# Kernel tuning notes

Hardware: AMD Instinct MI355X
Metric: run time of the kernel (lower is better)

The kernel has to match this reference:

```python
import jax, jax.numpy as jnp
import numpy as np

B, C, H, W = 2, 48, 128, 256
HEADS = 3
EPS_LN = 1e-6
EPS_NRM = 1e-12


def _conv(x, w, b, padding=0, dilation=1, groups=1):
    # x: NCHW, w: OIHW
    out = jax.lax.conv_general_dilated(
        x, w, window_strides=(1, 1),
        padding=[(padding, padding), (padding, padding)],
        rhs_dilation=(dilation, dilation),
        feature_group_count=groups,
        dimension_numbers=('NCHW', 'OIHW', 'NCHW'))
    return out + b[None, :, None, None]


def _ln2d(x, w, b):
    # LayerNorm over channel dim per pixel (NAFNet-style LayerNorm2d)
    mu = x.mean(axis=1, keepdims=True)
    var = ((x - mu) ** 2).mean(axis=1, keepdims=True)
    return (x - mu) / jnp.sqrt(var + EPS_LN) * w[None, :, None, None] + b[None, :, None, None]


def _l2norm(x):
    # F.normalize(dim=-1): x / max(||x||_2, eps)
    n = jnp.sqrt((x * x).sum(-1, keepdims=True))
    return x / jnp.maximum(n, EPS_NRM)


def setup_inputs() -> dict:
    key = jax.random.key(0)
    ks = iter(jax.random.split(key, 40))
    def nrm(shape, s=0.02):
        return jax.random.normal(next(ks), shape, jnp.float32) * s
    d = {
        'x_l': jax.random.normal(next(ks), (B, C, H, W), jnp.float32),
        'x_r': jax.random.normal(next(ks), (B, C, H, W), jnp.float32),
        'ln1_w': jnp.ones((C,), jnp.float32), 'ln1_b': jnp.zeros((C,), jnp.float32),
        'ln2_w': jnp.ones((C,), jnp.float32), 'ln2_b': jnp.zeros((C,), jnp.float32),
        'qkv_l_w': nrm((3 * C, C, 1, 1)), 'qkv_l_b': jnp.zeros((3 * C,), jnp.float32),
        'qkv_r_w': nrm((3 * C, C, 1, 1)), 'qkv_r_b': jnp.zeros((3 * C,), jnp.float32),
        'dw_l_w': nrm((3 * C, 1, 3, 3)), 'dw_l_b': jnp.zeros((3 * C,), jnp.float32),
        'dw_r_w': nrm((3 * C, 1, 3, 3)), 'dw_r_b': jnp.zeros((3 * C,), jnp.float32),
        'dil0_w': nrm((2 * C, 2 * C, 3, 3)), 'dil0_b': jnp.zeros((2 * C,), jnp.float32),
        'dil1_w': nrm((2 * C, 2 * C, 3, 3)), 'dil1_b': jnp.zeros((2 * C,), jnp.float32),
        'dil2_w': nrm((2 * C, 2 * C, 3, 3)), 'dil2_b': jnp.zeros((2 * C,), jnp.float32),
        'convQ_w': nrm((C, 6 * C, 1, 1)), 'convQ_b': jnp.zeros((C,), jnp.float32),
        'conv1_w': nrm((C, C, 1, 1)), 'conv1_b': jnp.zeros((C,), jnp.float32),
        'conv2_w': nrm((C, C, 1, 1)), 'conv2_b': jnp.zeros((C,), jnp.float32),
        'temperature': jnp.ones((HEADS, 1, 1), jnp.float32),
    }
    return d


def reference(x_l, x_r, ln1_w, ln1_b, ln2_w, ln2_b,
              qkv_l_w, qkv_l_b, qkv_r_w, qkv_r_b,
              dw_l_w, dw_l_b, dw_r_w, dw_r_b,
              dil0_w, dil0_b, dil1_w, dil1_b, dil2_w, dil2_b,
              convQ_w, convQ_b, conv1_w, conv1_b, conv2_w, conv2_b,
              temperature):
    b, c, h, w = x_l.shape
    hw = h * w
    ch = c // HEADS  # channels per head

    norm_l = _ln2d(x_l, ln1_w, ln1_b)
    norm_r = _ln2d(x_r, ln2_w, ln2_b)

    qkvl = _conv(_conv(norm_l, qkv_l_w, qkv_l_b), dw_l_w, dw_l_b, padding=1, groups=3 * c)
    qkvr = _conv(_conv(norm_r, qkv_r_w, qkv_r_b), dw_r_w, dw_r_b, padding=1, groups=3 * c)
    Q_l, K_l, V_l = jnp.split(qkvl, 3, axis=1)
    Q_r, K_r, V_r = jnp.split(qkvr, 3, axis=1)

    Q = jnp.concatenate((Q_l, Q_r), axis=1)  # [b, 2c, h, w]
    Q = jnp.concatenate((
        _conv(Q, dil0_w, dil0_b, padding=2, dilation=2),
        _conv(Q, dil1_w, dil1_b, padding=4, dilation=4),
        _conv(Q, dil2_w, dil2_b, padding=6, dilation=6)), axis=1)  # [b, 6c, h, w]
    Q = _conv(Q, convQ_w, convQ_b)  # [b, c, h, w]

    def heads(t):
        return t.reshape(b, HEADS, ch, hw)

    Q = _l2norm(heads(Q))
    K_l = _l2norm(heads(K_l))
    K_r = _l2norm(heads(K_r))
    V_l = heads(V_l)
    V_r = heads(V_r)

    # channel attention: [b, head, ch, ch]
    A_r2l = jax.nn.softmax(jnp.einsum('bhcn,bhdn->bhcd', Q, K_r) * temperature, axis=-1)
    A_l2r = jax.nn.softmax(jnp.einsum('bhcn,bhdn->bhcd', Q, K_l) * temperature, axis=-1)

    F_l = jnp.einsum('bhcd,bhdn->bhcn', A_r2l, V_l).reshape(b, c, h, w)
    F_r = jnp.einsum('bhcd,bhdn->bhcn', A_l2r, V_r).reshape(b, c, h, w)

    F_l = _conv(F_l, conv1_w, conv1_b)
    F_r = _conv(F_r, conv2_w, conv2_b)
    return (x_l + F_l, x_r + F_r)
```

## Files before the change

kernel.cpp:

```cpp
#include <hip/hip_runtime.h>
#include <hip/hip_bf16.h>

typedef __hip_bfloat16 bf16;
typedef __attribute__((ext_vector_type(8))) short short8;
typedef __attribute__((ext_vector_type(4))) float f32x4;
typedef unsigned int u32;

constexpr int IMG_H = 128;
constexpr int IMG_W = 256;
constexpr int HW    = IMG_H * IMG_W;
constexpr int BB    = 2;
constexpr int CC    = 48;
constexpr int C3    = 144;
constexpr int XPW   = 268;
constexpr int XOFF  = 6;
constexpr int QCP   = 104;
constexpr int QCS   = XPW * QCP;
constexpr int QCH   = QCS / 2;
constexpr int QCCH  = QCS / 8;

constexpr int WO_QKVL_W = 0;
constexpr int WO_QKVR_W = 6912;
constexpr int WO_DWL_W  = 13824;
constexpr int WO_DWR_W  = 15120;
constexpr int WO_C1_W   = 16416;
constexpr int WO_C2_W   = 18720;
constexpr int WO_QKVL_B = 21024;
constexpr int WO_QKVR_B = 21168;
constexpr int WO_DWL_B  = 21312;
constexpr int WO_DWR_B  = 21456;
constexpr int WO_C1_B   = 21600;
constexpr int WO_C2_B   = 21648;
constexpr int WO_LN1W   = 21696;
constexpr int WO_LN1B   = 21744;
constexpr int WO_LN2W   = 21792;
constexpr int WO_LN2B   = 21840;
constexpr int WO_TEMP   = 21888;
constexpr int WO_WQ     = 21952;
constexpr int WO_D0W    = 35776;
constexpr int WO_BQ     = 284608;
constexpr int WO_B0     = 284656;
constexpr int WO_B1     = 284752;
constexpr int WO_B2     = 284848;
constexpr int WO_WPACK  = 284944;
constexpr int WO_EFFB   = 409360;
constexpr int WO_AR2L   = 409712;
constexpr int WO_AL2R   = 411248;
constexpr int WO_M1     = 412800;
constexpr int WO_M2     = 417408;
constexpr int WO_WQP    = 422016;
constexpr int WO_PART   = 431232;
constexpr int WO_PART2  = WO_D0W;

constexpr size_t ACT_BASE_BYTES = 2118144;

constexpr size_t A_P  = 0;
constexpr size_t A_Q1 = 9437184;
constexpr size_t A_Q2 = 18874368;
constexpr size_t A_QC = 28311552;

constexpr int NPREP = 22;
struct PrepArgs {
  const void* src[NPREP];
  int dst[NPREP];
  int n[NPREP];
  int cstart[NPREP];
};

__device__ __forceinline__ bool probe_bf16(const void* ln1w) {
  return ((const unsigned short*)ln1w)[0] == 0x3F80;
}

__global__ __launch_bounds__(256) void prep_k(PrepArgs a, float* __restrict__ wsf) {
  bool isb = probe_bf16(a.src[12]);
  int chunk = blockIdx.x;
  int t = 0;
#pragma unroll 1
  while (t < NPREP - 1 && chunk >= a.cstart[t + 1]) ++t;
  int i = (chunk - a.cstart[t]) * 256 + threadIdx.x;
  if (i < a.n[t]) {
    float v = isb ? __bfloat162float(((const bf16*)a.src[t])[i])
                  : ((const float*)a.src[t])[i];
    wsf[a.dst[t] + i] = v;
  }
}

__global__ __launch_bounds__(512) void effw2_k(
    const float* __restrict__ wsf, const void* __restrict__ dwa,
    const void* __restrict__ dwb, const void* __restrict__ dwc,
    const void* __restrict__ probe, bf16* __restrict__ wpack) {
  int d  = blockIdx.x / 96;
  int ci = blockIdx.x % 96;
  __shared__ float wds[864];
  __shared__ float wqs[48 * 97];
  const void* dwp = (d == 0) ? dwa : (d == 1) ? dwb : dwc;
  bool isb = probe_bf16(probe);
  for (int idx = threadIdx.x; idx < 864; idx += 512) {
    int m = idx / 9, tt = idx % 9;
    int e = (m * 96 + ci) * 9 + tt;
    wds[idx] = isb ? __bfloat162float(((const bf16*)dwp)[e])
                   : ((const float*)dwp)[e];
  }
  for (int idx = threadIdx.x; idx < 4608; idx += 512) {
    int co = idx / 96, m = idx % 96;
    wqs[co * 97 + m] = wsf[WO_WQ + co * 288 + d * 96 + m];
  }
  __syncthreads();
  int tco = threadIdx.x;
  if (tco < 432) {
    int t = tco / 48, co = tco % 48;
    float s = 0.f;
#pragma unroll 8
    for (int m = 0; m < 96; ++m) s += wqs[co * 97 + m] * wds[m * 9 + t];
    int trow = t / 3, dxi = t % 3;
    int ti = (trow == 0) ? (2 - d) * 3 + dxi
           : (trow == 1) ? 9 + d * 3 + dxi
                         : 18 + d * 3 + dxi;
    int kc = ci >> 5, j = ci & 7;
    int L = ((ci & 31) >> 3) * 16 + (co & 15);
    int nt = co >> 4;
    int f = (ti * 3 + kc) * 3 + nt;
    wpack[(size_t)f * 512 + L * 8 + j] = __float2bfloat16(s);
  }
}

__global__ __launch_bounds__(256) void wqp_k(const float* __restrict__ wsf,
                                             bf16* __restrict__ wqp,
                                             float* __restrict__ effb) {
  if (blockIdx.x == 72) {
    int co = threadIdx.x;
    if (co < 48) {
      float s = wsf[WO_BQ + co];
      for (int m = 0; m < 96; ++m) {
        s += wsf[WO_WQ + co * 288 + m]       * wsf[WO_B0 + m];
        s += wsf[WO_WQ + co * 288 + 96 + m]  * wsf[WO_B1 + m];
        s += wsf[WO_WQ + co * 288 + 192 + m] * wsf[WO_B2 + m];
      }
      effb[co] = s;
    }
    return;
  }
  int idx = blockIdx.x * 256 + threadIdx.x;
  if (idx >= 18432) return;
  int side = idx / 9216;
  int rem = idx % 9216;
  int nt = rem / 1024;
  int kt = (rem / 512) % 2;
  int e  = rem % 512;
  int L = e >> 3, j = e & 7;
  int o = nt * 16 + (L & 15);
  int kp = kt * 32 + (L >> 4) * 8 + j;
  int g = kp >> 4, r = kp & 15;
  float val = 0.f;
  if (r < 12) {
    int c = g * 12 + r;
    val = wsf[(side ? WO_QKVR_W : WO_QKVL_W) + o * 48 + c];
  }
  wqp[idx] = __float2bfloat16(val);
}

__global__ __launch_bounds__(256) void lnqkv_k(
    const void* __restrict__ x, const void* __restrict__ probe,
    const float* __restrict__ lnw, const float* __restrict__ lnb,
    const bf16* __restrict__ wqp_side, const float* __restrict__ qb,
    bf16* __restrict__ pre) {
  __shared__ __align__(16) unsigned char LDSU[21504 + 18432];
  bf16* XNs = (bf16*)LDSU;
  float2* red = (float2*)(LDSU + 9216);
  bf16* Cs = (bf16*)LDSU;
  bf16* W = (bf16*)(LDSU + 21504);
  int tid = threadIdx.x;
  for (int i = tid; i < 1152; i += 256)
    ((uint4*)W)[i] = ((const uint4*)wqp_side)[i];

  int px = tid & 63;
  int w = tid >> 6;
  int p = blockIdx.x * 64 + px;
  int b = p >> 15;
  int pix = p & (HW - 1);
  size_t base = (size_t)b * CC * HW + pix;
  float v[12];
  if (probe_bf16(probe)) {
    const bf16* xp = (const bf16*)x + base;
#pragma unroll
    for (int c = 0; c < 12; ++c)
      v[c] = __bfloat162float(xp[(size_t)(w * 12 + c) * HW]);
  } else {
    const float* xp = (const float*)x + base;
#pragma unroll
    for (int c = 0; c < 12; ++c) v[c] = xp[(size_t)(w * 12 + c) * HW];
  }
  float s = 0.f, s2 = 0.f;
#pragma unroll
  for (int c = 0; c < 12; ++c) { s += v[c]; s2 += v[c] * v[c]; }
  red[w * 64 + px] = make_float2(s, s2);
  __syncthreads();
  float S = 0.f, S2 = 0.f;
#pragma unroll
  for (int i = 0; i < 4; ++i) {
    float2 r2 = red[i * 64 + px];
    S += r2.x; S2 += r2.y;
  }
  float mu = S * (1.f / 48.f);
  float var = S2 * (1.f / 48.f) - mu * mu;
  float rs = rsqrtf(var + 1e-6f);
  bf16 o16[16];
#pragma unroll
  for (int c = 0; c < 12; ++c)
    o16[c] = __float2bfloat16((v[c] - mu) * rs * lnw[w * 12 + c] + lnb[w * 12 + c]);
#pragma unroll
  for (int c = 12; c < 16; ++c) o16[c] = __float2bfloat16(0.f);
  *(uint4*)(XNs + px * 72 + w * 16) = *(uint4*)(o16);
  *(uint4*)(XNs + px * 72 + w * 16 + 8) = *(uint4*)(o16 + 8);
  __syncthreads();

  int L = tid & 63;
  int lo = L & 15, hi = L >> 4;
  const bf16* arow = XNs + (size_t)(w * 16 + lo) * 72 + hi * 8;
  short8 a0 = *(const short8*)(arow);
  short8 a1 = *(const short8*)(arow + 32);
  __syncthreads();
#pragma unroll
  for (int nt = 0; nt < 9; ++nt) {
    float bvv = qb[nt * 16 + lo];
    f32x4 acc = {bvv, bvv, bvv, bvv};
    acc = __builtin_amdgcn_mfma_f32_16x16x32_bf16(
        a0, *(const short8*)(W + (nt * 2 + 0) * 512 + L * 8), acc, 0, 0, 0);
    acc = __builtin_amdgcn_mfma_f32_16x16x32_bf16(
        a1, *(const short8*)(W + (nt * 2 + 1) * 512 + L * 8), acc, 0, 0, 0);
#pragma unroll
    for (int r = 0; r < 4; ++r)
      Cs[(nt * 16 + lo) * 66 + w * 16 + hi * 4 + r] = __float2bfloat16(acc[r]);
  }
  __syncthreads();
  int pix0 = (blockIdx.x * 64) & (HW - 1);
#pragma unroll
  for (int pass = 0; pass < 18; ++pass) {
    int o = pass * 8 + (tid >> 5);
    int px2 = (tid & 31) * 2;
    bf16 t2[2];
    t2[0] = Cs[o * 66 + px2];
    t2[1] = Cs[o * 66 + px2 + 1];
    *(unsigned*)(pre + ((size_t)(b * C3 + o)) * HW + pix0 + px2) = *(unsigned*)t2;
  }
}

__global__ __launch_bounds__(256) void dw_k(
    const bf16* __restrict__ in, const float* __restrict__ w9,
    const float* __restrict__ bias, bf16* __restrict__ out) {
  int gid = blockIdx.x;
  int yt = gid & 15;
  int c = (gid >> 4) % C3;
  int b = gid / (16 * C3);
  int ry = threadIdx.x >> 5, xi = threadIdx.x & 31;
  int y = yt * 8 + ry;
  int x0 = xi * 8;
  const bf16* base = in + ((size_t)(b * C3 + c)) * HW;
  float wv[9];
#pragma unroll
  for (int t = 0; t < 9; ++t) wv[t] = w9[c * 9 + t];
  float bz = bias[c];
  float acc[8];
#pragma unroll
  for (int i = 0; i < 8; ++i) acc[i] = bz;
#pragma unroll
  for (int ky = 0; ky < 3; ++ky) {
    int yy = y + ky - 1;
    if ((unsigned)yy >= (unsigned)IMG_H) continue;
    const bf16* row = base + yy * IMG_W + x0;
    uint4 m = *(const uint4*)(row);
    float f[10];
    f[0] = (x0 > 0) ? __bfloat162float(row[-1]) : 0.f;
    f[9] = (x0 + 8 < IMG_W) ? __bfloat162float(row[8]) : 0.f;
    f[1] = __uint_as_float(m.x << 16);
    f[2] = __uint_as_float(m.x & 0xFFFF0000u);
    f[3] = __uint_as_float(m.y << 16);
    f[4] = __uint_as_float(m.y & 0xFFFF0000u);
    f[5] = __uint_as_float(m.z << 16);
    f[6] = __uint_as_float(m.z & 0xFFFF0000u);
    f[7] = __uint_as_float(m.w << 16);
    f[8] = __uint_as_float(m.w & 0xFFFF0000u);
    float w0 = wv[ky * 3], w1 = wv[ky * 3 + 1], w2 = wv[ky * 3 + 2];
#pragma unroll
    for (int i = 0; i < 8; ++i)
      acc[i] += w0 * f[i] + w1 * f[i + 1] + w2 * f[i + 2];
  }
  bf16 o[8];
#pragma unroll
  for (int i = 0; i < 8; ++i) o[i] = __float2bfloat16(acc[i]);
  *(uint4*)(out + ((size_t)(b * C3 + c)) * HW + y * IMG_W + x0) = *(uint4*)o;
}

__global__ __launch_bounds__(256) void qc_k(const bf16* __restrict__ q1,
                                            const bf16* __restrict__ q2,
                                            bf16* __restrict__ qc) {
  int b = blockIdx.x >> 7;
  int y = blockIdx.x & 127;
  int half = blockIdx.y;
  int tid = threadIdx.x;
  int x0 = half * 128;
  int px = tid & 127;
  int cig = tid >> 7;
  __shared__ __align__(16) bf16 T[128][100];
#pragma unroll 8
  for (int k = 0; k < 48; ++k) {
    int ci = cig * 48 + k;
    const bf16* src = (ci < 48)
        ? q1 + (((size_t)(b * C3 + ci)) * IMG_H + y) * IMG_W
        : q2 + (((size_t)(b * C3 + ci - 48)) * IMG_H + y) * IMG_W;
    T[px][ci] = src[x0 + px];
  }
  __syncthreads();
  size_t rowbase = ((size_t)(b * IMG_H + y)) * QCS;
#pragma unroll 1
  for (int i = 0; i < 14; ++i) {
    int e4 = i * 256 + tid;
    if (e4 >= QCH / 4) break;
    int e = e4 * 4 + half * QCH;
    int xp = e / QCP;
    int cin = e % QCP;
    int x = xp - XOFF;
    uint2 val;
    val.x = 0u; val.y = 0u;
    if ((unsigned)x < (unsigned)IMG_W && cin < 96) {
      val = *(const uint2*)(&T[x - x0][cin]);
    }
    *(uint2*)(qc + rowbase + e) = val;
  }
}

__global__ __launch_bounds__(512, 2) void dil_mfma_k(
    const bf16* __restrict__ qc, const bf16* __restrict__ wp,
    const float* __restrict__ effb, bf16* __restrict__ qh) {
  __shared__ __align__(16) unsigned char LDSU[55744 + 18432];
  bf16* Arow = (bf16*)LDSU;
  bf16* Wb   = (bf16*)(LDSU + 55744);
  float* Cs  = (float*)LDSU;

  int bid = blockIdx.x;
  int xcd = bid & 7;
  int rest = bid >> 3;
  int y = xcd * 16 + (rest & 15);
  int b = rest >> 4;
  int tid = threadIdx.x;
  int L = tid & 63;
  int w = tid >> 6;
  int lo = L & 15, hi = L >> 4;

  f32x4 acc[2][3];
#pragma unroll
  for (int g2 = 0; g2 < 2; ++g2)
#pragma unroll
    for (int nt = 0; nt < 3; ++nt) {
      float bv = effb[nt * 16 + lo];
      acc[g2][nt] = {bv, bv, bv, bv};
    }

#pragma unroll
  for (int k = 0; k < 2; ++k) {
    int c = w + k * 8;
    if (c < 9) {
      __builtin_amdgcn_global_load_lds(
          (const __attribute__((address_space(1))) u32*)(wp + c * 512 + L * 8),
          (__attribute__((address_space(3))) u32*)(Wb + c * 512 + L * 8),
          16, 0, 0);
    }
  }

  int dy_prev = -100;
#pragma unroll 1
  for (int g = 0; g < 9; ++g) {
    int D = (g < 3) ? (6 - 2 * g) : (g < 6) ? (2 * (g - 2)) : (2 * (g - 5));
    int dy = (g < 3) ? -D : (g < 6) ? 0 : D;
    int yy = y + dy;
    bool valid = (unsigned)yy < (unsigned)IMG_H;
    if (valid && dy != dy_prev) {
      __syncthreads();
      const bf16* src = qc + (size_t)(b * IMG_H + yy) * QCS;
#pragma unroll
      for (int r = 0; r < 7; ++r) {
        int c = w + r * 8;
        int i = c * 64 + L;
        if (i < QCCH) {
          __builtin_amdgcn_global_load_lds(
              (const __attribute__((address_space(1))) u32*)(src + (size_t)i * 8),
              (__attribute__((address_space(3))) u32*)(Arow + (size_t)c * 512),
              16, 0, 0);
        }
      }
      __syncthreads();
      dy_prev = dy;
    }
#pragma unroll
    for (int dxi = 0; dxi < 3; ++dxi) {
      int ti = g * 3 + dxi;
      if (ti < 26) {
        const bf16* srcw = wp + (ti + 1) * 4608;
        bf16* dstw = Wb + ((ti + 1) & 1) * 4608;
#pragma unroll
        for (int k = 0; k < 2; ++k) {
          int c = w + k * 8;
          if (c < 9) {
            __builtin_amdgcn_global_load_lds(
                (const __attribute__((address_space(1))) u32*)(srcw + c * 512 + L * 8),
                (__attribute__((address_space(3))) u32*)(dstw + c * 512 + L * 8),
                16, 0, 0);
          }
        }
      }
      if (valid) {
        const bf16* wb = Wb + (ti & 1) * 4608;
        int dx = (dxi - 1) * D;
        const bf16* ar = Arow + (size_t)(XOFF + dx + w * 32 + lo) * QCP + hi * 8;
#pragma unroll
        for (int g2 = 0; g2 < 2; ++g2)
#pragma unroll
          for (int kc = 0; kc < 3; ++kc) {
            short8 a = *(const short8*)(ar + g2 * (16 * QCP) + kc * 32);
#pragma unroll
            for (int nt = 0; nt < 3; ++nt)
              acc[g2][nt] = __builtin_amdgcn_mfma_f32_16x16x32_bf16(
                  a, *(const short8*)(wb + (kc * 3 + nt) * 512 + L * 8),
                  acc[g2][nt], 0, 0, 0);
          }
      }
      __syncthreads();
    }
  }

#pragma unroll
  for (int g2 = 0; g2 < 2; ++g2)
#pragma unroll
    for (int nt = 0; nt < 3; ++nt)
#pragma unroll
      for (int r = 0; r < 4; ++r)
        Cs[(nt * 16 + lo) * 260 + w * 32 + g2 * 16 + hi * 4 + r] = acc[g2][nt][r];
  __syncthreads();
  size_t obase = (size_t)b * CC * HW + (size_t)y * IMG_W;
#pragma unroll
  for (int i = 0; i < 6; ++i) {
    int chunk = i * 512 + tid;
    int co = chunk >> 6;
    int px4 = (chunk & 63) * 4;
    const float* s = Cs + co * 260 + px4;
    bf16 t4[4];
    t4[0] = __float2bfloat16(s[0]);
    t4[1] = __float2bfloat16(s[1]);
    t4[2] = __float2bfloat16(s[2]);
    t4[3] = __float2bfloat16(s[3]);
    *(uint2*)(qh + obase + (size_t)co * HW + px4) = *(uint2*)t4;
  }
}

__device__ __forceinline__ float blo(unsigned u) {
  return __uint_as_float(u << 16);
}
__device__ __forceinline__ float bhi(unsigned u) {
  return __uint_as_float(u & 0xFFFF0000u);
}

__global__ __launch_bounds__(256) void logits_mfma_k(
    const bf16* __restrict__ qh, const bf16* __restrict__ qkvl,
    const bf16* __restrict__ qkvr, float* __restrict__ part,
    float* __restrict__ part2) {
  int abh = blockIdx.x;
  int chunk = blockIdx.y;
  int a = abh / 6;
  int b = (abh / 3) % 2;
  int h = abh % 3;
  int tid = threadIdx.x;
  int L = tid & 63, w = tid >> 6;
  int lo = L & 15, hi = L >> 4;
  const bf16* qrow = qh + ((size_t)(b * CC + h * 16 + lo)) * HW;
  const bf16* krow =
      ((a == 0) ? qkvr : qkvl) + ((size_t)(b * C3 + 48 + h * 16 + lo)) * HW;
  int px0 = chunk * 1024 + w * 256 + hi * 8;
  f32x4 acc = {0.f, 0.f, 0.f, 0.f};
  float aq = 0.f, ak = 0.f;
#pragma unroll
  for (int s = 0; s < 8; ++s) {
    short8 av = *(const short8*)(qrow + px0 + s * 32);
    short8 bv = *(const short8*)(krow + px0 + s * 32);
    acc = __builtin_amdgcn_mfma_f32_16x16x32_bf16(av, bv, acc, 0, 0, 0);
#pragma unroll
    for (int j = 0; j < 4; ++j) {
      u32 ua = ((const u32*)&av)[j];
      u32 ub = ((const u32*)&bv)[j];
      float q0 = blo(ua), q1 = bhi(ua);
      float k0 = blo(ub), k1 = bhi(ub);
      aq += q0 * q0 + q1 * q1;
      ak += k0 * k0 + k1 * k1;
    }
  }
  __shared__ float red[4][256];
  __shared__ float sq[256], sk[256];
#pragma unroll
  for (int r = 0; r < 4; ++r) red[w][(hi * 4 + r) * 16 + lo] = acc[r];
  sq[tid] = aq;
  sk[tid] = ak;
  __syncthreads();
  float sum = red[0][tid] + red[1][tid] + red[2][tid] + red[3][tid];
  part[((size_t)abh * 32 + chunk) * 256 + tid] = sum;
  if (tid < 32) {
    const float* srcr = (tid < 16) ? sq : sk;
    int lo2 = tid & 15;
    float s = 0.f;
#pragma unroll
    for (int w2 = 0; w2 < 4; ++w2)
#pragma unroll
      for (int h2 = 0; h2 < 4; ++h2) s += srcr[w2 * 64 + h2 * 16 + lo2];
    part2[((size_t)abh * 32 + chunk) * 32 + tid] = s;
  }
}

__global__ __launch_bounds__(256) void logits_red_k(
    const float* __restrict__ part, const float* __restrict__ part2,
    const float* __restrict__ temp, float* __restrict__ logr2l,
    float* __restrict__ logl2r) {
  int abh = blockIdx.x;
  int a = abh / 6, h = abh % 3;
  int bnum = (abh / 3) % 2;
  int t = threadIdx.x;
  int i = t >> 4, j = t & 15;
  __shared__ float nrm[32];
  if (t < 32) {
    float s = 0.f;
    const float* p2 = part2 + (size_t)abh * 32 * 32 + t;
#pragma unroll 8
    for (int c = 0; c < 32; ++c) s += p2[c * 32];
    nrm[t] = fmaxf(sqrtf(s), 1e-12f);
  }
  float s = 0.f;
  const float* p = part + (size_t)abh * 32 * 256 + t;
#pragma unroll 8
  for (int c = 0; c < 32; ++c) s += p[c * 256];
  __syncthreads();
  float val = s / (nrm[i] * nrm[16 + j]) * temp[h];
  ((a == 0) ? logr2l : logl2r)[bnum * 768 + h * 256 + i * 16 + j] = val;
}

__global__ __launch_bounds__(256) void softmaxM_k(float* __restrict__ wsf) {
  int tid = threadIdx.x;
  __shared__ float A1[1536], A2[1536];
  if (tid < 192) {
    const float* p = wsf + ((tid < 96) ? WO_AR2L : WO_AL2R) + (tid % 96) * 16;
    float* dst = ((tid < 96) ? A1 : A2) + (tid % 96) * 16;
    float m = -1e30f;
#pragma unroll
    for (int j = 0; j < 16; ++j) m = fmaxf(m, p[j]);
    float s = 0.f;
    float e[16];
#pragma unroll
    for (int j = 0; j < 16; ++j) {
      e[j] = expf(p[j] - m);
      s += e[j];
    }
    float inv = 1.f / s;
#pragma unroll
    for (int j = 0; j < 16; ++j) dst[j] = e[j] * inv;
  }
  __syncthreads();
#pragma unroll 1
  for (int idx = tid; idx < 4608; idx += 256) {
    int b = idx / 2304;
    int r = idx % 2304;
    int o = r / 48;
    int cp = r % 48;
    int h = cp >> 4, j = cp & 15;
    const float* a1 = &A1[((b * 3 + h) * 16) * 16 + j];
    const float* a2 = &A2[((b * 3 + h) * 16) * 16 + j];
    float s1 = 0.f, s2 = 0.f;
#pragma unroll
    for (int i = 0; i < 16; ++i) {
      s1 += wsf[WO_C1_W + o * 48 + h * 16 + i] * a1[i * 16];
      s2 += wsf[WO_C2_W + o * 48 + h * 16 + i] * a2[i * 16];
    }
    wsf[WO_M1 + idx] = s1;
    wsf[WO_M2 + idx] = s2;
  }
}

__global__ __launch_bounds__(256) void attn_out2_k(
    const bf16* __restrict__ q1, const bf16* __restrict__ q2,
    const void* __restrict__ x1, const void* __restrict__ x2,
    const void* __restrict__ probe, const float* __restrict__ Mall,
    const float* __restrict__ cball, void* __restrict__ out) {
  int side = blockIdx.y;
  const bf16* qkv = side ? q2 : q1;
  const void* x = side ? x2 : x1;
  const float* M = Mall + side * 4608;
  const float* cb = cball + side * 48;
  int tid = threadIdx.x;
  int p = blockIdx.x * 256 + tid;
  int b = __builtin_amdgcn_readfirstlane(p >> 15);
  int pix = p & (HW - 1);
  bool isb = probe_bf16(probe);

  float v[CC];
  const bf16* vb = qkv + ((size_t)(b * C3 + 96)) * HW + pix;
#pragma unroll
  for (int c = 0; c < CC; ++c) v[c] = __bfloat162float(vb[(size_t)c * HW]);

  const float* Mb = M + b * 2304;
  size_t base = (size_t)b * CC * HW + pix;
  size_t obase = (size_t)side * BB * CC * HW + base;
  if (isb) {
    const bf16* xp = (const bf16*)x + base;
    bf16* op = (bf16*)out + obase;
#pragma unroll 4
    for (int o = 0; o < CC; ++o) {
      float acc = cb[o];
      const float* mrow = Mb + o * 48;
#pragma unroll
      for (int c = 0; c < CC; ++c) acc += mrow[c] * v[c];
      op[(size_t)o * HW] =
          __float2bfloat16(acc + __bfloat162float(xp[(size_t)o * HW]));
    }
  } else {
    const float* xp = (const float*)x + base;
    float* op = (float*)out + obase;
#pragma unroll 4
    for (int o = 0; o < CC; ++o) {
      float acc = cb[o];
      const float* mrow = Mb + o * 48;
#pragma unroll
      for (int c = 0; c < CC; ++c) acc += mrow[c] * v[c];
      op[(size_t)o * HW] = acc + xp[(size_t)o * HW];
    }
  }
}

extern "C" void kernel_launch(void* const* d_in, const int* in_sizes, int n_in,
                              void* d_out, int out_size, void* d_ws, size_t ws_size,
                              hipStream_t stream) {
  (void)in_sizes; (void)n_in; (void)out_size; (void)ws_size;
  const void* x_l = d_in[0];
  const void* x_r = d_in[1];
  const void* probe = d_in[2];
  float* wsf = (float*)d_ws;
  bf16* wpack = (bf16*)(wsf + WO_WPACK);
  bf16* wqp = (bf16*)(wsf + WO_WQP);
  bf16* act = (bf16*)((char*)d_ws + ACT_BASE_BYTES);
  bf16* P  = act + A_P;
  bf16* Q1 = act + A_Q1;
  bf16* Q2 = act + A_Q2;
  bf16* QC = act + A_QC;
  bf16* qh = P;

  PrepArgs pa;
  const int srcIdx[NPREP] = {6, 8, 10, 12, 22, 24, 7, 9, 11, 13, 23, 25,
                             2, 3, 4, 5, 26, 20, 21, 15, 17, 19};
  const int dstOff[NPREP] = {WO_QKVL_W, WO_QKVR_W, WO_DWL_W, WO_DWR_W, WO_C1_W,
                             WO_C2_W, WO_QKVL_B, WO_QKVR_B, WO_DWL_B, WO_DWR_B,
                             WO_C1_B, WO_C2_B, WO_LN1W, WO_LN1B, WO_LN2W,
                             WO_LN2B, WO_TEMP, WO_WQ, WO_BQ, WO_B0, WO_B1, WO_B2};
  const int ns[NPREP] = {6912, 6912, 1296, 1296, 2304, 2304, 144, 144, 144, 144,
                         48, 48, 48, 48, 48, 48, 3, 13824, 48, 96, 96, 96};
  int ck = 0;
  for (int i = 0; i < NPREP; ++i) {
    pa.src[i] = d_in[srcIdx[i]];
    pa.dst[i] = dstOff[i];
    pa.n[i] = ns[i];
    pa.cstart[i] = ck;
    ck += (ns[i] + 255) / 256;
  }
  prep_k<<<ck, 256, 0, stream>>>(pa, wsf);

  effw2_k<<<288, 512, 0, stream>>>(wsf, d_in[14], d_in[16], d_in[18],
                                   probe, wpack);
  wqp_k<<<73, 256, 0, stream>>>(wsf, wqp, wsf + WO_EFFB);

  lnqkv_k<<<1024, 256, 0, stream>>>(x_l, probe, wsf + WO_LN1W, wsf + WO_LN1B,
                                    wqp, wsf + WO_QKVL_B, P);
  dw_k<<<BB * C3 * 16, 256, 0, stream>>>(P, wsf + WO_DWL_W, wsf + WO_DWL_B, Q1);
  lnqkv_k<<<1024, 256, 0, stream>>>(x_r, probe, wsf + WO_LN2W, wsf + WO_LN2B,
                                    wqp + 9216, wsf + WO_QKVR_B, P);
  dw_k<<<BB * C3 * 16, 256, 0, stream>>>(P, wsf + WO_DWR_W, wsf + WO_DWR_B, Q2);

  qc_k<<<dim3(BB * IMG_H, 2), 256, 0, stream>>>(Q1, Q2, QC);

  dil_mfma_k<<<256, 512, 0, stream>>>(QC, wpack, wsf + WO_EFFB, qh);

  logits_mfma_k<<<dim3(12, 32), 256, 0, stream>>>(qh, Q1, Q2, wsf + WO_PART,
                                                  wsf + WO_PART2);
  logits_red_k<<<12, 256, 0, stream>>>(wsf + WO_PART, wsf + WO_PART2,
                                       wsf + WO_TEMP, wsf + WO_AR2L,
                                       wsf + WO_AL2R);
  softmaxM_k<<<1, 256, 0, stream>>>(wsf);

  attn_out2_k<<<dim3(256, 2), 256, 0, stream>>>(
      Q1, Q2, x_l, x_r, probe, wsf + WO_M1, wsf + WO_C1_B, d_out);
}
```

Measured before the change: 278.1 us.

## Double-buffer per-row-offset weight groups to cut barriers in dilated conv

The dilated-conv MFMA kernel now prefetches the weights for all three dx taps of a row offset at once, in a larger double buffer. Before, it loaded one tap at a time. This cuts the number of __syncthreads per row group from roughly four to one and shares each weight fragment load across both pixel groups. The cost is more LDS (about 111 KB), which drops launch bounds from two blocks per CU to one and lowers occupancy.

```diff
diff --git a/kernel.cpp b/kernel.cpp
--- a/kernel.cpp
+++ b/kernel.cpp
@@ -329,13 +329,15 @@
   }
 }
 
-__global__ __launch_bounds__(512, 2) void dil_mfma_k(
+__global__ __launch_bounds__(512, 1) void dil_mfma_k(
     const bf16* __restrict__ qc, const bf16* __restrict__ wp,
     const float* __restrict__ effb, bf16* __restrict__ qh) {
-  __shared__ __align__(16) unsigned char LDSU[55744 + 18432];
+  __shared__ __align__(16) unsigned char LDSU[111040];
   bf16* Arow = (bf16*)LDSU;
-  bf16* Wb   = (bf16*)(LDSU + 55744);
+  bf16* Wg   = (bf16*)(LDSU + 55744);
   float* Cs  = (float*)LDSU;
+  constexpr int WGE = 13824;
+  constexpr int WGC = WGE / 8;
 
   int bid = blockIdx.x;
   int xcd = bid & 7;
@@ -357,12 +359,12 @@
     }
 
 #pragma unroll
-  for (int k = 0; k < 2; ++k) {
-    int c = w + k * 8;
-    if (c < 9) {
+  for (int r = 0; r < 4; ++r) {
+    int i = r * 512 + tid;
+    if (i < WGC) {
       __builtin_amdgcn_global_load_lds(
-          (const __attribute__((address_space(1))) u32*)(wp + c * 512 + L * 8),
-          (__attribute__((address_space(3))) u32*)(Wb + c * 512 + L * 8),
+          (const __attribute__((address_space(1))) u32*)(wp + (size_t)i * 8),
+          (__attribute__((address_space(3))) u32*)(Wg + (size_t)i * 8),
           16, 0, 0);
     }
   }
@@ -379,55 +381,56 @@
       const bf16* src = qc + (size_t)(b * IMG_H + yy) * QCS;
 #pragma unroll
       for (int r = 0; r < 7; ++r) {
-        int c = w + r * 8;
-        int i = c * 64 + L;
+        int i = r * 512 + tid;
         if (i < QCCH) {
           __builtin_amdgcn_global_load_lds(
               (const __attribute__((address_space(1))) u32*)(src + (size_t)i * 8),
-              (__attribute__((address_space(3))) u32*)(Arow + (size_t)c * 512),
+              (__attribute__((address_space(3))) u32*)(Arow + (size_t)i * 8),
               16, 0, 0);
         }
       }
-      __syncthreads();
       dy_prev = dy;
     }
-#pragma unroll
-    for (int dxi = 0; dxi < 3; ++dxi) {
-      int ti = g * 3 + dxi;
-      if (ti < 26) {
-        const bf16* srcw = wp + (ti + 1) * 4608;
-        bf16* dstw = Wb + ((ti + 1) & 1) * 4608;
-#pragma unroll
-        for (int k = 0; k < 2; ++k) {
-          int c = w + k * 8;
-          if (c < 9) {
-            __builtin_amdgcn_global_load_lds(
-                (const __attribute__((address_space(1))) u32*)(srcw + c * 512 + L * 8),
-                (__attribute__((address_space(3))) u32*)(dstw + c * 512 + L * 8),
-                16, 0, 0);
+    __syncthreads();
+    if (g < 8) {
+      const bf16* srcw = wp + (size_t)(g + 1) * WGE;
+      bf16* dstw = Wg + ((g + 1) & 1) * WGE;
+#pragma unroll
+      for (int r = 0; r < 4; ++r) {
+        int i = r * 512 + tid;
+        if (i < WGC) {
+          __builtin_amdgcn_global_load_lds(
+              (const __attribute__((address_space(1))) u32*)(srcw + (size_t)i * 8),
+              (__attribute__((address_space(3))) u32*)(dstw + (size_t)i * 8),
+              16, 0, 0);
+        }
+      }
+    }
+    if (valid) {
+      const bf16* wgb = Wg + (g & 1) * WGE;
+#pragma unroll
+      for (int dxi = 0; dxi < 3; ++dxi) {
+        int dx = (dxi - 1) * D;
+        const bf16* ar = Arow + (size_t)(XOFF + dx + w * 32 + lo) * QCP + hi * 8;
+        const bf16* wb = wgb + dxi * 4608 + L * 8;
+#pragma unroll
+        for (int kc = 0; kc < 3; ++kc) {
+          short8 a0 = *(const short8*)(ar + kc * 32);
+          short8 a1 = *(const short8*)(ar + 16 * QCP + kc * 32);
+#pragma unroll
+          for (int nt = 0; nt < 3; ++nt) {
+            short8 wv = *(const short8*)(wb + (kc * 3 + nt) * 512);
+            acc[0][nt] = __builtin_amdgcn_mfma_f32_16x16x32_bf16(
+                a0, wv, acc[0][nt], 0, 0, 0);
+            acc[1][nt] = __builtin_amdgcn_mfma_f32_16x16x32_bf16(
+                a1, wv, acc[1][nt], 0, 0, 0);
           }
         }
       }
-      if (valid) {
-        const bf16* wb = Wb + (ti & 1) * 4608;
-        int dx = (dxi - 1) * D;
-        const bf16* ar = Arow + (size_t)(XOFF + dx + w * 32 + lo) * QCP + hi * 8;
-#pragma unroll
-        for (int g2 = 0; g2 < 2; ++g2)
-#pragma unroll
-          for (int kc = 0; kc < 3; ++kc) {
-            short8 a = *(const short8*)(ar + g2 * (16 * QCP) + kc * 32);
-#pragma unroll
-            for (int nt = 0; nt < 3; ++nt)
-              acc[g2][nt] = __builtin_amdgcn_mfma_f32_16x16x32_bf16(
-                  a, *(const short8*)(wb + (kc * 3 + nt) * 512 + L * 8),
-                  acc[g2][nt], 0, 0, 0);
-          }
-      }
-      __syncthreads();
-    }
-  }
-
+    }
+  }
+
+  __syncthreads();
 #pragma unroll
   for (int g2 = 0; g2 < 2; ++g2)
 #pragma unroll
```

New measurement: 275.6 us. About the same (-0.9%).
